# Kernel optimization log

Hardware: AMD Instinct MI355X
Metric: run time of the kernel (lower is better)

## Reference

```python
import jax, jax.numpy as jnp
import numpy as np

S = 10        # spiking_segment_count
TEMP = 50.0

def setup_inputs() -> dict:
    key = jax.random.key(0)
    ks = jax.random.split(key, 6)
    bs, din, dout = 2048, 1024, 1024
    x = jax.random.normal(ks[0], (bs, din), dtype=jnp.float32)
    t = jax.random.uniform(ks[1], (bs,), dtype=jnp.float32)  # in [0,1) subset of [-1,1]
    scale = 1.0 / np.sqrt(din)
    param_W = jax.random.normal(ks[2], (din, dout * S * 3), dtype=jnp.float32) * scale
    param_b = jax.random.normal(ks[3], (dout * S * 3,), dtype=jnp.float32) * 0.01
    norm_W = jax.random.normal(ks[4], (din, dout), dtype=jnp.float32) * scale
    norm_b = jax.random.normal(ks[5], (dout,), dtype=jnp.float32) * 0.01
    return {"x": x, "t": t, "param_W": param_W, "param_b": param_b,
            "norm_W": norm_W, "norm_b": norm_b}

def reference(x, t, param_W, param_b, norm_W, norm_b):
    bs = x.shape[0]
    dout = norm_W.shape[1]
    # param GEMM -> (bs, S, dout, 3)
    params = (x @ param_W + param_b).reshape(bs, S, dout, 3)
    weights = jax.nn.softmax(params[..., 0], axis=1)                 # (bs, S, dout)
    keypoints = jnp.concatenate(
        [jnp.zeros_like(weights[:, :1]), jnp.cumsum(weights, axis=1)], axis=1
    ) * 2.0 - 1.0                                                    # (bs, S+1, dout)
    slopes = jnp.tanh(params[..., 1])
    intercepts = params[..., 2]
    tt = t.reshape(-1, 1, 1)                                         # (bs, 1, 1)
    starts = keypoints[:, :S]
    ends = keypoints[:, 1:]
    residual = slopes * tt + intercepts                              # (bs, S, dout)
    validity = ((tt >= starts) & (tt < ends)) | ((tt == 1.0) & (ends == 1.0))
    vf = validity.astype(x.dtype)
    left_margin = jnp.sum((tt - starts) * vf, axis=1)                # (bs, dout)
    right_margin = jnp.sum((ends - tt) * vf, axis=1)
    lw = jax.nn.sigmoid(-TEMP * left_margin)
    rw = jax.nn.sigmoid(-TEMP * right_margin)
    lv = jnp.concatenate([vf[:, :1], vf[:, :-1]], axis=1)
    rv = jnp.concatenate([vf[:, 1:], vf[:, -1:]], axis=1)
    sw = -(lw + rw - 1.0)
    result = (lw * jnp.sum(residual * lv, axis=1)
              + sw * jnp.sum(residual * vf, axis=1)
              + rw * jnp.sum(residual * rv, axis=1))
    # norm == 'constant': subtract segment-wise integral, add norm_net(x)
    integral = jnp.sum(0.5 * slopes * (ends * ends - starts * starts)
                       + intercepts * weights, axis=1) * 0.5
    norm_target = x @ norm_W + norm_b
    return result - integral + norm_target
```

## Files before the change

kernel.cpp:

```cpp
#include <hip/hip_runtime.h>
#include <cstdint>
#include <cstddef>

#define BS    2048
#define DIN   1024
#define DOUT  1024
#define SSEG  10
#define NPAR  30720
#define NPK   20480
#define NCOL2 21504
#define NLG   10240
#define TAU   5e-5f
#define WL_CAP 1048576u

#define NB_SPLIT 2048
#define NB_NORM  1024
#define NB_TRW   2560

#define GEMM_BLKS 992

typedef _Float16 half_t;
typedef __attribute__((ext_vector_type(8))) _Float16 half8;
typedef __attribute__((ext_vector_type(4))) _Float16 half4;
typedef __attribute__((ext_vector_type(2))) _Float16 half2v;
typedef __attribute__((ext_vector_type(4))) float   floatx4;

__device__ __forceinline__ void gload16(const void* g, void* l) {
  __builtin_amdgcn_global_load_lds(
      (const __attribute__((address_space(1))) void*)g,
      (__attribute__((address_space(3))) void*)l, 16, 0, 0);
}

__global__ void k_zero(unsigned* c) { if (threadIdx.x == 0) *c = 0; }

__global__ __launch_bounds__(256) void k_prep(const float* __restrict__ x,
                                              half_t* __restrict__ xh,
                                              half_t* __restrict__ xl,
                                              const float* __restrict__ nW,
                                              const float* __restrict__ pW,
                                              half_t* __restrict__ wsm,
                                              half_t* __restrict__ wh,
                                              half_t* __restrict__ wlo,
                                              float* __restrict__ wlt,
                                              unsigned* __restrict__ cnt) {
  __shared__ float tile[32][384];
  int bid = blockIdx.x;
  int tid = threadIdx.x;

  if (bid < NB_SPLIT) {
    if (bid == 0 && tid == 0) *cnt = 0;
    int i = bid * 256 + tid;
    floatx4 v = ((const floatx4*)x)[i];
    half4 h, l;
    #pragma unroll
    for (int c = 0; c < 4; c++) { h[c] = (half_t)v[c]; l[c] = (half_t)(v[c] - (float)h[c]); }
    ((half4*)xh)[i] = h;
    ((half4*)xl)[i] = l;
    return;
  }

  if (bid < NB_SPLIT + NB_NORM) {
    int b2 = bid - NB_SPLIT;
    int col0 = (b2 & 31) * 32;
    int k0   = (b2 >> 5) * 32;
    int tx = tid & 31;
    int ty = tid >> 5;
    float* t33 = &tile[0][0];
    #pragma unroll
    for (int r = ty; r < 32; r += 8)
      t33[r * 33 + tx] = nW[(size_t)(k0 + r) * DOUT + col0 + tx];
    __syncthreads();
    #pragma unroll
    for (int r = ty; r < 32; r += 8)
      wsm[(size_t)(col0 + r + NPK) * DIN + k0 + tx] = (half_t)t33[tx * 33 + r];
    return;
  }

  int b3 = bid - NB_SPLIT - NB_NORM;
  int bx = b3 % 80;
  int k0 = (b3 / 80) * 32;
  int s  = bx >> 3;
  int d0 = (bx & 7) * 128;

  const float* sb = pW + (size_t)k0 * NPAR + bx * 384;
  for (int i = tid; i < 32 * 96; i += 256) {
    int r = i / 96, q = i - r * 96;
    ((floatx4*)&tile[r][0])[q] = ((const floatx4*)(sb + (size_t)r * NPAR))[q];
  }
  __syncthreads();

  for (int ci = tid; ci < 3072; ci += 256) {
    if (ci < 1024) {
      int rl = ci >> 2, kc = ci & 3;
      int jj = rl >> 1, cbit = rl & 1;
      int col = 3 * jj + 1 + cbit;
      half8 v;
      #pragma unroll
      for (int m = 0; m < 8; m++) v[m] = (half_t)tile[kc * 8 + m][col];
      *(half8*)(wsm + (size_t)(s * 2048 + 2 * (d0 + jj) + cbit) * DIN + k0 + kc * 8) = v;
    } else if (ci < 1536) {
      int u = ci - 1024;
      int jj = u >> 2, kc = u & 3;
      half8 v;
      #pragma unroll
      for (int m = 0; m < 8; m++) v[m] = (half_t)(tile[kc * 8 + m][3 * jj] * 32.0f);
      *(half8*)(wh + (size_t)(s * 1024 + d0 + jj) * DIN + k0 + kc * 8) = v;
    } else if (ci < 2048) {
      int u = ci - 1536;
      int jj = u >> 2, kc = u & 3;
      half8 v;
      #pragma unroll
      for (int m = 0; m < 8; m++) {
        float raw = tile[kc * 8 + m][3 * jj] * 32.0f;
        half_t h = (half_t)raw;
        v[m] = (half_t)(raw - (float)h);
      }
      *(half8*)(wlo + (size_t)(s * 1024 + d0 + jj) * DIN + k0 + kc * 8) = v;
    } else {
      int u = ci - 2048;
      int jj = u >> 3, kc = u & 7;
      floatx4 v;
      #pragma unroll
      for (int m = 0; m < 4; m++) v[m] = tile[kc * 4 + m][3 * jj];
      *(floatx4*)(wlt + (size_t)(s * 1024 + d0 + jj) * DIN + k0 + kc * 4) = v;
    }
  }
}

__global__ __launch_bounds__(512, 2) void k_gemm2(
    const half_t* __restrict__ xh, const half_t* __restrict__ xl,
    const half_t* __restrict__ wh, const half_t* __restrict__ wlo,
    const half_t* __restrict__ wsm,
    float* __restrict__ Lg, half_t* __restrict__ P,
    const float* __restrict__ pb, const float* __restrict__ nb) {
  __shared__ __attribute__((aligned(128))) char lds[131072];

  int bid = blockIdx.x;
  int tid = threadIdx.x;
  int w = tid >> 6, l = tid & 63;
  int wr = w >> 2, wc = w & 3;
  int l15 = l & 15, quad = l >> 4;

  int mode, mt, nt;
  if (bid < 320) { mode = 0; mt = bid & 7; nt = bid >> 3; }
  else { int s2 = bid - 320; mode = 1; mt = s2 & 7; nt = s2 >> 3; }
  int m0 = mt * 256, n0 = nt * 256;

  int sp = (l & 7) ^ ((l >> 3) & 7);
  int srowA = m0 + w * 32 + 2 * (l >> 3) + (sp >> 2);
  int srowB = n0 + w * 32 + 2 * (l >> 3) + (sp >> 2);
  int scol = (sp & 3) * 8;

  int lofs = (l15 >> 1) * 128 + (((((l15 & 1) << 2) | quad) ^ (l15 >> 1)) << 4);

  floatx4 acc[8][4] = {};

  if (mode == 0) {
    auto stage0 = [&](int c) {
      char* base = lds + ((c & 1) * 65536) + w * 2048;
      const half_t* ga = xh + (size_t)srowA * DIN + c * 32 + scol;
      const half_t* gx = xl + (size_t)srowA * DIN + c * 32 + scol;
      const half_t* gh = wh + (size_t)srowB * DIN + c * 32 + scol;
      const half_t* gl = wlo + (size_t)srowB * DIN + c * 32 + scol;
      gload16(ga, base);                gload16(ga + 16 * DIN, base + 1024);
      gload16(gx, base + 16384);        gload16(gx + 16 * DIN, base + 16384 + 1024);
      gload16(gh, base + 32768);        gload16(gh + 16 * DIN, base + 32768 + 1024);
      gload16(gl, base + 49152);        gload16(gl + 16 * DIN, base + 49152 + 1024);
    };

    stage0(0);
    asm volatile("s_waitcnt vmcnt(0)" ::: "memory");
    __builtin_amdgcn_s_barrier();

    for (int c = 0; c < 32; ++c) {
      const char* base = lds + (c & 1) * 65536;
      const char* aXH = base + wr * 8192 + lofs;
      const char* aXL = base + 16384 + wr * 8192 + lofs;
      const char* bWH = base + 32768 + wc * 4096 + lofs;
      const char* bWL = base + 49152 + wc * 4096 + lofs;
      if (c + 1 < 32) stage0(c + 1);

      half8 bh[4], bl[4], a0[4], a1[4], x0[4], x1[4];
      #pragma unroll
      for (int ni = 0; ni < 4; ni++) bh[ni] = *(const half8*)(bWH + ni * 1024);
      #pragma unroll
      for (int mi = 0; mi < 4; mi++) a0[mi] = *(const half8*)(aXH + mi * 1024);
      #pragma unroll
      for (int mi = 0; mi < 4; mi++) a1[mi] = *(const half8*)(aXH + 4096 + mi * 1024);
      #pragma unroll
      for (int mi = 0; mi < 4; mi++)
        #pragma unroll
        for (int ni = 0; ni < 4; ni++) {
          acc[mi][ni]     = __builtin_amdgcn_mfma_f32_16x16x32_f16(a0[mi], bh[ni], acc[mi][ni], 0, 0, 0);
          acc[4 + mi][ni] = __builtin_amdgcn_mfma_f32_16x16x32_f16(a1[mi], bh[ni], acc[4 + mi][ni], 0, 0, 0);
        }
      #pragma unroll
      for (int mi = 0; mi < 4; mi++) x0[mi] = *(const half8*)(aXL + mi * 1024);
      #pragma unroll
      for (int mi = 0; mi < 4; mi++) x1[mi] = *(const half8*)(aXL + 4096 + mi * 1024);
      #pragma unroll
      for (int mi = 0; mi < 4; mi++)
        #pragma unroll
        for (int ni = 0; ni < 4; ni++) {
          acc[mi][ni]     = __builtin_amdgcn_mfma_f32_16x16x32_f16(x0[mi], bh[ni], acc[mi][ni], 0, 0, 0);
          acc[4 + mi][ni] = __builtin_amdgcn_mfma_f32_16x16x32_f16(x1[mi], bh[ni], acc[4 + mi][ni], 0, 0, 0);
        }
      #pragma unroll
      for (int ni = 0; ni < 4; ni++) bl[ni] = *(const half8*)(bWL + ni * 1024);
      #pragma unroll
      for (int mi = 0; mi < 4; mi++)
        #pragma unroll
        for (int ni = 0; ni < 4; ni++) {
          acc[mi][ni]     = __builtin_amdgcn_mfma_f32_16x16x32_f16(a0[mi], bl[ni], acc[mi][ni], 0, 0, 0);
          acc[4 + mi][ni] = __builtin_amdgcn_mfma_f32_16x16x32_f16(a1[mi], bl[ni], acc[4 + mi][ni], 0, 0, 0);
        }
      if (c + 1 < 32) {
        __builtin_amdgcn_sched_barrier(0);
        asm volatile("s_waitcnt vmcnt(0)" ::: "memory");
        __builtin_amdgcn_s_barrier();
      }
    }
  } else {
    auto stage1 = [&](int kt) {
      char* base = lds + ((kt & 3) * 32768) + w * 2048;
      const half_t* ga = xh + (size_t)srowA * DIN + kt * 32 + scol;
      const half_t* gb = wsm + (size_t)srowB * DIN + kt * 32 + scol;
      gload16(ga, base);            gload16(ga + 16 * DIN, base + 1024);
      gload16(gb, base + 16384);    gload16(gb + 16 * DIN, base + 16384 + 1024);
    };

    stage1(0); stage1(1); stage1(2);
    asm volatile("s_waitcnt vmcnt(8)" ::: "memory");
    __builtin_amdgcn_s_barrier();

    for (int kt = 0; kt < 32; ++kt) {
      const char* base = lds + (kt & 3) * 32768;
      const char* a = base + wr * 8192 + lofs;
      const char* b = base + 16384 + wc * 4096 + lofs;
      if (kt + 3 < 32) stage1(kt + 3);

      half8 bf[4], af[4], ag[4];
      #pragma unroll
      for (int ni = 0; ni < 4; ni++) bf[ni] = *(const half8*)(b + ni * 1024);
      #pragma unroll
      for (int mi = 0; mi < 4; mi++) af[mi] = *(const half8*)(a + mi * 1024);
      #pragma unroll
      for (int mi = 0; mi < 4; mi++) ag[mi] = *(const half8*)(a + 4096 + mi * 1024);
      #pragma unroll
      for (int mi = 0; mi < 4; mi++)
        #pragma unroll
        for (int ni = 0; ni < 4; ni++) {
          acc[mi][ni]     = __builtin_amdgcn_mfma_f32_16x16x32_f16(af[mi], bf[ni], acc[mi][ni], 0, 0, 0);
          acc[4 + mi][ni] = __builtin_amdgcn_mfma_f32_16x16x32_f16(ag[mi], bf[ni], acc[4 + mi][ni], 0, 0, 0);
        }
      if (kt < 29) {
        __builtin_amdgcn_sched_barrier(0);
        asm volatile("s_waitcnt vmcnt(8)" ::: "memory");
        __builtin_amdgcn_s_barrier();
      } else if (kt == 29) {
        __builtin_amdgcn_sched_barrier(0);
        asm volatile("s_waitcnt vmcnt(4)" ::: "memory");
        __builtin_amdgcn_s_barrier();
      } else if (kt == 30) {
        __builtin_amdgcn_sched_barrier(0);
        asm volatile("s_waitcnt vmcnt(0)" ::: "memory");
        __builtin_amdgcn_s_barrier();
      }
    }
  }

  int rbase = m0 + wr * 128 + quad * 4;
  int cbase = n0 + wc * 64 + l15;
  if (mode == 0) {
    #pragma unroll
    for (int ni = 0; ni < 4; ni++) {
      int col = cbase + ni * 16;
      float bias = pb[(col >> 10) * 3072 + (col & 1023) * 3];
      #pragma unroll
      for (int mi = 0; mi < 8; mi++) {
        int row = rbase + mi * 16;
        floatx4 v = acc[mi][ni];
        #pragma unroll
        for (int r = 0; r < 4; r++)
          Lg[(size_t)(row + r) * NLG + col] = v[r] * 0.03125f + bias;
      }
    }
  } else {
    #pragma unroll
    for (int ni = 0; ni < 4; ni++) {
      int col = cbase + ni * 16;
      float bias;
      if (col < NPK) {
        int s = col >> 11, rem = col & 2047;
        bias = pb[s * 3072 + 3 * (rem >> 1) + 1 + (rem & 1)];
      } else {
        bias = nb[col - NPK];
      }
      #pragma unroll
      for (int mi = 0; mi < 8; mi++) {
        int row = rbase + mi * 16;
        floatx4 v = acc[mi][ni];
        #pragma unroll
        for (int r = 0; r < 4; r++)
          P[(size_t)(row + r) * NCOL2 + col] = (half_t)(v[r] + bias);
      }
    }
  }
}

__device__ __forceinline__ float spiking_eval(const float* p, float tt, float* mind) {
  float mx = -1e30f;
  #pragma unroll
  for (int s = 0; s < SSEG; s++) mx = fmaxf(mx, p[3 * s]);
  float ew[10], wsum = 0.0f;
  #pragma unroll
  for (int s = 0; s < SSEG; s++) { ew[s] = __expf(p[3 * s] - mx); wsum += ew[s]; }
  float inv = 1.0f / wsum;

  float kp[11];
  kp[0] = -1.0f;
  float cum = 0.0f, md = 1e30f;
  #pragma unroll
  for (int s = 0; s < SSEG; s++) {
    cum += ew[s] * inv;
    kp[s + 1] = cum * 2.0f - 1.0f;
    md = fminf(md, fabsf(tt - kp[s + 1]));
  }
  *mind = md;

  float vf[10], resid[10];
  float lm = 0.0f, rm = 0.0f, integ = 0.0f;
  #pragma unroll
  for (int s = 0; s < SSEG; s++) {
    float p1 = p[3 * s + 1], p2 = p[3 * s + 2];
    float e2 = __expf(2.0f * fabsf(p1));
    float th = copysignf(1.0f - 2.0f / (e2 + 1.0f), p1);
    resid[s] = th * tt + p2;
    float st = kp[s], en = kp[s + 1];
    bool v = ((tt >= st) && (tt < en)) || ((tt == 1.0f) && (en == 1.0f));
    float vv = v ? 1.0f : 0.0f;
    vf[s] = vv;
    lm += (tt - st) * vv;
    rm += (en - tt) * vv;
    integ += 0.5f * th * (en * en - st * st) + p2 * (ew[s] * inv);
  }
  float resLV = 0.0f, resV = 0.0f, resRV = 0.0f;
  #pragma unroll
  for (int s = 0; s < SSEG; s++) {
    float lv = (s == 0) ? vf[0] : vf[s - 1];
    float rv = (s == 9) ? vf[9] : vf[s + 1];
    resLV += resid[s] * lv;
    resV  += resid[s] * vf[s];
    resRV += resid[s] * rv;
  }
  float lw = 1.0f / (1.0f + __expf(50.0f * lm));
  float rw = 1.0f / (1.0f + __expf(50.0f * rm));
  float swt = 1.0f - lw - rw;
  return lw * resLV + swt * resV + rw * resRV - 0.5f * integ + p[30];
}

__global__ __launch_bounds__(256) void k_pointwise(const half_t* __restrict__ P,
                                                   const float* __restrict__ Lg,
                                                   const float* __restrict__ t,
                                                   float* __restrict__ out,
                                                   unsigned* __restrict__ cnt,
                                                   unsigned* __restrict__ wl,
                                                   unsigned cap) {
  __shared__ __attribute__((aligned(16))) half_t sp[SSEG * 512];
  int b = blockIdx.x, dg = blockIdx.y, tid = threadIdx.x;
  const half_t* Pb = P + (size_t)b * NCOL2;
  for (int i = tid; i < SSEG * 64; i += 256) {
    int s = i >> 6, e = i & 63;
    ((uint4*)sp)[(s << 6) + e] = ((const uint4*)(Pb + s * 2048 + dg * 512))[e];
  }
  float tt = t[b];
  float nt = (float)Pb[NPK + dg * 256 + tid];
  const float* Lb = Lg + (size_t)b * NLG + dg * 256 + tid;
  __syncthreads();

  float p[31];
  #pragma unroll
  for (int s = 0; s < SSEG; s++) {
    p[3 * s] = Lb[s * 1024];
    half2v hv = ((const half2v*)sp)[s * 256 + tid];
    p[3 * s + 1] = (float)hv.x;
    p[3 * s + 2] = (float)hv.y;
  }
  p[30] = nt;
  float mind;
  float r = spiking_eval(p, tt, &mind);
  int d = dg * 256 + tid;
  out[(size_t)b * DOUT + d] = r;
  if (wl != nullptr && mind < TAU) {
    unsigned idx = atomicAdd(cnt, 1u);
    if (idx < cap) wl[idx] = ((unsigned)b << 10) | (unsigned)d;
  }
}

__global__ __launch_bounds__(256) void k_naive(const float* __restrict__ x,
                                               const float* __restrict__ t,
                                               const float* __restrict__ pW,
                                               const float* __restrict__ pb,
                                               const float* __restrict__ nW,
                                               const float* __restrict__ nb,
                                               float* __restrict__ out,
                                               unsigned* __restrict__ cnt,
                                               unsigned* __restrict__ wl,
                                               unsigned cap) {
  __shared__ float xs[DIN];
  int b = blockIdx.x, dg = blockIdx.y, tid = threadIdx.x;
  for (int i = tid; i < DIN; i += 256) xs[i] = x[(size_t)b * DIN + i];
  __syncthreads();
  int d = dg * 256 + tid;
  float acc[31];
  #pragma unroll
  for (int i = 0; i < 31; i++) acc[i] = 0.0f;
  for (int k = 0; k < DIN; k++) {
    float xv = xs[k];
    const float* wr = pW + (size_t)k * NPAR + 3 * d;
    #pragma unroll
    for (int s = 0; s < SSEG; s++) {
      acc[3 * s]     += xv * wr[s * 3072];
      acc[3 * s + 1] += xv * wr[s * 3072 + 1];
      acc[3 * s + 2] += xv * wr[s * 3072 + 2];
    }
    acc[30] += xv * nW[(size_t)k * DOUT + d];
  }
  #pragma unroll
  for (int s = 0; s < SSEG; s++) {
    acc[3 * s]     += pb[s * 3072 + 3 * d];
    acc[3 * s + 1] += pb[s * 3072 + 3 * d + 1];
    acc[3 * s + 2] += pb[s * 3072 + 3 * d + 2];
  }
  acc[30] += nb[d];
  float mind;
  float r = spiking_eval(acc, t[b], &mind);
  out[(size_t)b * DOUT + d] = r;
  if (wl != nullptr && mind < TAU) {
    unsigned idx = atomicAdd(cnt, 1u);
    if (idx < cap) wl[idx] = ((unsigned)b << 10) | (unsigned)d;
  }
}

__global__ __launch_bounds__(256) void k_redo(const float* __restrict__ x,
                                              const float* __restrict__ t,
                                              const float* __restrict__ pW,
                                              const float* __restrict__ pb,
                                              const float* __restrict__ nW,
                                              const float* __restrict__ nb,
                                              const half_t* __restrict__ P,
                                              const float* __restrict__ WLt,
                                              int haveP,
                                              const unsigned* __restrict__ cnt,
                                              const unsigned* __restrict__ wl,
                                              unsigned cap,
                                              float* __restrict__ out) {
  unsigned n = *cnt;
  if (n > cap) n = cap;
  int lane = threadIdx.x & 63;
  unsigned wave = (blockIdx.x * 256 + threadIdx.x) >> 6;
  unsigned nwaves = (gridDim.x * 256) >> 6;

  for (unsigned e = wave; e < n; e += nwaves) {
    unsigned code = wl[e];
    int b = (int)(code >> 10), d = (int)(code & 1023);

    double lg[10], sl[10], ic[10], nt = 0.0;
    #pragma unroll
    for (int s = 0; s < SSEG; s++) { lg[s] = 0.0; sl[s] = 0.0; ic[s] = 0.0; }

    if (haveP) {
      for (int k = lane; k < DIN; k += 64) {
        double xv = (double)x[(size_t)b * DIN + k];
        #pragma unroll
        for (int s = 0; s < SSEG; s++)
          lg[s] += xv * (double)WLt[(size_t)(s * 1024 + d) * DIN + k];
      }
    } else {
      for (int k = lane; k < DIN; k += 64) {
        double xv = (double)x[(size_t)b * DIN + k];
        const float* wr = pW + (size_t)k * NPAR + 3 * d;
        #pragma unroll
        for (int s = 0; s < SSEG; s++) {
          lg[s] += xv * (double)wr[s * 3072];
          sl[s] += xv * (double)wr[s * 3072 + 1];
          ic[s] += xv * (double)wr[s * 3072 + 2];
        }
        nt += xv * (double)nW[(size_t)k * DOUT + d];
      }
    }
    #pragma unroll
    for (int off = 32; off > 0; off >>= 1) {
      #pragma unroll
      for (int s = 0; s < SSEG; s++) lg[s] += __shfl_down(lg[s], off);
      if (!haveP) {
        #pragma unroll
        for (int s = 0; s < SSEG; s++) {
          sl[s] += __shfl_down(sl[s], off);
          ic[s] += __shfl_down(ic[s], off);
        }
        nt += __shfl_down(nt, off);
      }
    }

    if (lane == 0) {
      double slope[10], icpt[10], ntv;
      if (haveP) {
        const half_t* Pr = P + (size_t)b * NCOL2;
        #pragma unroll
        for (int s = 0; s < SSEG; s++) {
          slope[s] = tanh((double)(float)Pr[s * 2048 + 2 * d]);
          icpt[s]  = (double)(float)Pr[s * 2048 + 2 * d + 1];
        }
        ntv = (double)(float)Pr[NPK + d];
      } else {
        #pragma unroll
        for (int s = 0; s < SSEG; s++) {
          slope[s] = tanh(sl[s] + (double)pb[s * 3072 + 3 * d + 1]);
          icpt[s]  = ic[s] + (double)pb[s * 3072 + 3 * d + 2];
        }
        ntv = nt + (double)nb[d];
      }
      #pragma unroll
      for (int s = 0; s < SSEG; s++) lg[s] += (double)pb[s * 3072 + 3 * d];

      double mx = -1e300;
      #pragma unroll
      for (int s = 0; s < SSEG; s++) mx = fmax(mx, lg[s]);
      double ew[10], ws = 0.0;
      #pragma unroll
      for (int s = 0; s < SSEG; s++) { ew[s] = exp(lg[s] - mx); ws += ew[s]; }

      double kp[11];
      kp[0] = -1.0;
      double cum = 0.0;
      #pragma unroll
      for (int s = 0; s < SSEG; s++) { cum += ew[s] / ws; kp[s + 1] = cum * 2.0 - 1.0; }

      double tt = (double)t[b];
      double vf[10], resid[10], lm = 0.0, rm = 0.0, integ = 0.0;
      #pragma unroll
      for (int s = 0; s < SSEG; s++) {
        double st = kp[s], en = kp[s + 1];
        bool v = ((tt >= st) && (tt < en)) || ((tt == 1.0) && (en == 1.0));
        double vv = v ? 1.0 : 0.0;
        vf[s] = vv;
        resid[s] = slope[s] * tt + icpt[s];
        lm += (tt - st) * vv;
        rm += (en - tt) * vv;
        integ += 0.5 * slope[s] * (en * en - st * st) + icpt[s] * (ew[s] / ws);
      }
      double rLV = 0.0, rV = 0.0, rRV = 0.0;
      #pragma unroll
      for (int s = 0; s < SSEG; s++) {
        double lv = (s == 0) ? vf[0] : vf[s - 1];
        double rv = (s == 9) ? vf[9] : vf[s + 1];
        rLV += resid[s] * lv;
        rV  += resid[s] * vf[s];
        rRV += resid[s] * rv;
      }
      double lw = 1.0 / (1.0 + exp(50.0 * lm));
      double rw = 1.0 / (1.0 + exp(50.0 * rm));
      double res = lw * rLV + (1.0 - lw - rw) * rV + rw * rRV - 0.5 * integ + ntv;
      out[(size_t)b * DOUT + d] = (float)res;
    }
  }
}

extern "C" void kernel_launch(void* const* d_in, const int* in_sizes, int n_in,
                              void* d_out, int out_size, void* d_ws, size_t ws_size,
                              hipStream_t stream) {
  const float* x  = (const float*)d_in[0];
  const float* t  = (const float*)d_in[1];
  const float* pW = (const float*)d_in[2];
  const float* pb = (const float*)d_in[3];
  const float* nW = (const float*)d_in[4];
  const float* nb = (const float*)d_in[5];
  float* out = (float*)d_out;

  const size_t o_cnt = 0;
  const size_t o_wl  = 64;
  const size_t o_xh  = o_wl  + (size_t)WL_CAP * 4;
  const size_t o_xl  = o_xh  + (size_t)BS * DIN * 2;
  const size_t o_wsm = o_xl  + (size_t)BS * DIN * 2;
  const size_t o_wh  = o_wsm + (size_t)NCOL2 * DIN * 2;
  const size_t o_wlo = o_wh  + (size_t)NLG * DIN * 2;
  const size_t o_wlt = o_wlo + (size_t)NLG * DIN * 2;
  const size_t o_p   = o_wlt + (size_t)NLG * DIN * 4;
  const size_t o_lg  = o_p   + (size_t)BS * NCOL2 * 2;
  const size_t need  = o_lg  + (size_t)BS * NLG * 4;

  bool have_wl = ws_size >= 1024 * 1024;
  unsigned* cnt = (unsigned*)((char*)d_ws + o_cnt);
  unsigned* wl  = (unsigned*)((char*)d_ws + o_wl);
  unsigned cap  = 0;
  if (have_wl) {
    size_t avail = (ws_size >= need) ? (size_t)WL_CAP
                                     : (ws_size - o_wl) / 4;
    cap = (unsigned)(avail < WL_CAP ? avail : WL_CAP);
  }

  if (ws_size >= need) {
    half_t* xh  = (half_t*)((char*)d_ws + o_xh);
    half_t* xl  = (half_t*)((char*)d_ws + o_xl);
    half_t* wsm = (half_t*)((char*)d_ws + o_wsm);
    half_t* wh  = (half_t*)((char*)d_ws + o_wh);
    half_t* wlo = (half_t*)((char*)d_ws + o_wlo);
    float*  wlt = (float*)((char*)d_ws + o_wlt);
    half_t* P   = (half_t*)((char*)d_ws + o_p);
    float*  Lg  = (float*)((char*)d_ws + o_lg);

    k_prep<<<NB_SPLIT + NB_NORM + NB_TRW, 256, 0, stream>>>(x, xh, xl, nW, pW,
                                                            wsm, wh, wlo, wlt, cnt);
    k_gemm2<<<GEMM_BLKS, 512, 0, stream>>>(xh, xl, wh, wlo, wsm, Lg, P, pb, nb);
    k_pointwise<<<dim3(BS, DOUT / 256), 256, 0, stream>>>(P, Lg, t, out, cnt,
                                                          have_wl ? wl : nullptr, cap);
    if (have_wl)
      k_redo<<<256, 256, 0, stream>>>(x, t, pW, pb, nW, nb, P, wlt, 1, cnt, wl, cap, out);
  } else {
    if (have_wl) k_zero<<<1, 64, 0, stream>>>(cnt);
    k_naive<<<dim3(BS, DOUT / 256), 256, 0, stream>>>(x, t, pW, pb, nW, nb, out, cnt,
                                                      have_wl ? wl : nullptr, cap);
    if (have_wl)
      k_redo<<<256, 256, 0, stream>>>(x, t, pW, pb, nW, nb, nullptr, nullptr, 0,
                                      cnt, wl, cap, out);
  }
}
```

Before: 565.7 us.

## Interleave global prefetch with MFMA phases using barriers and setprio in GEMM loop

Splits each K-step of both GEMM modes into sub-phases. Each phase issues LDS fragment loads and part of the next tile's global-to-LDS prefetch, synchronises all waves with an s_barrier, then runs an MFMA cluster at raised wave priority via s_setprio. This spreads memory issue between compute bursts and keeps waves in lockstep, following the ping-pong scheduling pattern, with the aim of better overlap between loads and matrix work. The cost is several extra workgroup barriers per iteration, which could add stalls if the waves are already balanced.

```diff
diff --git a/kernel.cpp b/kernel.cpp
--- a/kernel.cpp
+++ b/kernel.cpp
@@ -156,19 +156,18 @@
   floatx4 acc[8][4] = {};
 
   if (mode == 0) {
-    auto stage0 = [&](int c) {
-      char* base = lds + ((c & 1) * 65536) + w * 2048;
-      const half_t* ga = xh + (size_t)srowA * DIN + c * 32 + scol;
-      const half_t* gx = xl + (size_t)srowA * DIN + c * 32 + scol;
-      const half_t* gh = wh + (size_t)srowB * DIN + c * 32 + scol;
-      const half_t* gl = wlo + (size_t)srowB * DIN + c * 32 + scol;
-      gload16(ga, base);                gload16(ga + 16 * DIN, base + 1024);
-      gload16(gx, base + 16384);        gload16(gx + 16 * DIN, base + 16384 + 1024);
-      gload16(gh, base + 32768);        gload16(gh + 16 * DIN, base + 32768 + 1024);
-      gload16(gl, base + 49152);        gload16(gl + 16 * DIN, base + 49152 + 1024);
-    };
-
-    stage0(0);
+    const half_t* gA = xh + (size_t)srowA * DIN + scol;
+    const half_t* gX = xl + (size_t)srowA * DIN + scol;
+    const half_t* gH = wh + (size_t)srowB * DIN + scol;
+    const half_t* gL = wlo + (size_t)srowB * DIN + scol;
+
+    {
+      char* base = lds + w * 2048;
+      gload16(gA, base);                gload16(gA + 16 * DIN, base + 1024);
+      gload16(gX, base + 16384);        gload16(gX + 16 * DIN, base + 16384 + 1024);
+      gload16(gH, base + 32768);        gload16(gH + 16 * DIN, base + 32768 + 1024);
+      gload16(gL, base + 49152);        gload16(gL + 16 * DIN, base + 49152 + 1024);
+    }
     asm volatile("s_waitcnt vmcnt(0)" ::: "memory");
     __builtin_amdgcn_s_barrier();
 
@@ -178,15 +177,25 @@
       const char* aXL = base + 16384 + wr * 8192 + lofs;
       const char* bWH = base + 32768 + wc * 4096 + lofs;
       const char* bWL = base + 49152 + wc * 4096 + lofs;
-      if (c + 1 < 32) stage0(c + 1);
-
-      half8 bh[4], bl[4], a0[4], a1[4], x0[4], x1[4];
+      bool pre = (c + 1 < 32);
+      char* sbase = lds + ((c + 1) & 1) * 65536 + w * 2048;
+      int ko = (c + 1) * 32;
+
+      half8 bh[4], a0[4], a1[4];
       #pragma unroll
       for (int ni = 0; ni < 4; ni++) bh[ni] = *(const half8*)(bWH + ni * 1024);
       #pragma unroll
       for (int mi = 0; mi < 4; mi++) a0[mi] = *(const half8*)(aXH + mi * 1024);
       #pragma unroll
       for (int mi = 0; mi < 4; mi++) a1[mi] = *(const half8*)(aXH + 4096 + mi * 1024);
+      if (pre) {
+        gload16(gA + ko, sbase);           gload16(gA + ko + 16 * DIN, sbase + 1024);
+        gload16(gX + ko, sbase + 16384);   gload16(gX + ko + 16 * DIN, sbase + 16384 + 1024);
+      }
+      __builtin_amdgcn_s_barrier();
+      asm volatile("s_waitcnt lgkmcnt(0)" ::: "memory");
+      __builtin_amdgcn_sched_barrier(0);
+      __builtin_amdgcn_s_setprio(1);
       #pragma unroll
       for (int mi = 0; mi < 4; mi++)
         #pragma unroll
@@ -194,10 +203,22 @@
           acc[mi][ni]     = __builtin_amdgcn_mfma_f32_16x16x32_f16(a0[mi], bh[ni], acc[mi][ni], 0, 0, 0);
           acc[4 + mi][ni] = __builtin_amdgcn_mfma_f32_16x16x32_f16(a1[mi], bh[ni], acc[4 + mi][ni], 0, 0, 0);
         }
+      __builtin_amdgcn_s_setprio(0);
+      __builtin_amdgcn_s_barrier();
+
+      half8 x0[4], x1[4];
       #pragma unroll
       for (int mi = 0; mi < 4; mi++) x0[mi] = *(const half8*)(aXL + mi * 1024);
       #pragma unroll
       for (int mi = 0; mi < 4; mi++) x1[mi] = *(const half8*)(aXL + 4096 + mi * 1024);
+      if (pre) {
+        gload16(gH + ko, sbase + 32768);   gload16(gH + ko + 16 * DIN, sbase + 32768 + 1024);
+        gload16(gL + ko, sbase + 49152);   gload16(gL + ko + 16 * DIN, sbase + 49152 + 1024);
+      }
+      __builtin_amdgcn_s_barrier();
+      asm volatile("s_waitcnt lgkmcnt(0)" ::: "memory");
+      __builtin_amdgcn_sched_barrier(0);
+      __builtin_amdgcn_s_setprio(1);
       #pragma unroll
       for (int mi = 0; mi < 4; mi++)
         #pragma unroll
@@ -205,8 +226,16 @@
           acc[mi][ni]     = __builtin_amdgcn_mfma_f32_16x16x32_f16(x0[mi], bh[ni], acc[mi][ni], 0, 0, 0);
           acc[4 + mi][ni] = __builtin_amdgcn_mfma_f32_16x16x32_f16(x1[mi], bh[ni], acc[4 + mi][ni], 0, 0, 0);
         }
+      __builtin_amdgcn_s_setprio(0);
+      __builtin_amdgcn_s_barrier();
+
+      half8 bl[4];
       #pragma unroll
       for (int ni = 0; ni < 4; ni++) bl[ni] = *(const half8*)(bWL + ni * 1024);
+      __builtin_amdgcn_s_barrier();
+      asm volatile("s_waitcnt lgkmcnt(0)" ::: "memory");
+      __builtin_amdgcn_sched_barrier(0);
+      __builtin_amdgcn_s_setprio(1);
       #pragma unroll
       for (int mi = 0; mi < 4; mi++)
         #pragma unroll
@@ -214,19 +243,20 @@
           acc[mi][ni]     = __builtin_amdgcn_mfma_f32_16x16x32_f16(a0[mi], bl[ni], acc[mi][ni], 0, 0, 0);
           acc[4 + mi][ni] = __builtin_amdgcn_mfma_f32_16x16x32_f16(a1[mi], bl[ni], acc[4 + mi][ni], 0, 0, 0);
         }
-      if (c + 1 < 32) {
+      __builtin_amdgcn_s_setprio(0);
+      if (pre) {
         __builtin_amdgcn_sched_barrier(0);
         asm volatile("s_waitcnt vmcnt(0)" ::: "memory");
         __builtin_amdgcn_s_barrier();
       }
     }
   } else {
+    const half_t* gA = xh + (size_t)srowA * DIN + scol;
+    const half_t* gB = wsm + (size_t)srowB * DIN + scol;
     auto stage1 = [&](int kt) {
       char* base = lds + ((kt & 3) * 32768) + w * 2048;
-      const half_t* ga = xh + (size_t)srowA * DIN + kt * 32 + scol;
-      const half_t* gb = wsm + (size_t)srowB * DIN + kt * 32 + scol;
-      gload16(ga, base);            gload16(ga + 16 * DIN, base + 1024);
-      gload16(gb, base + 16384);    gload16(gb + 16 * DIN, base + 16384 + 1024);
+      gload16(gA + kt * 32, base);            gload16(gA + kt * 32 + 16 * DIN, base + 1024);
+      gload16(gB + kt * 32, base + 16384);    gload16(gB + kt * 32 + 16 * DIN, base + 16384 + 1024);
     };
 
     stage1(0); stage1(1); stage1(2);
@@ -237,22 +267,38 @@
       const char* base = lds + (kt & 3) * 32768;
       const char* a = base + wr * 8192 + lofs;
       const char* b = base + 16384 + wc * 4096 + lofs;
+
+      half8 bf[4], af[4];
+      #pragma unroll
+      for (int ni = 0; ni < 4; ni++) bf[ni] = *(const half8*)(b + ni * 1024);
+      #pragma unroll
+      for (int mi = 0; mi < 4; mi++) af[mi] = *(const half8*)(a + mi * 1024);
       if (kt + 3 < 32) stage1(kt + 3);
-
-      half8 bf[4], af[4], ag[4];
-      #pragma unroll
-      for (int ni = 0; ni < 4; ni++) bf[ni] = *(const half8*)(b + ni * 1024);
-      #pragma unroll
-      for (int mi = 0; mi < 4; mi++) af[mi] = *(const half8*)(a + mi * 1024);
+      __builtin_amdgcn_s_barrier();
+      asm volatile("s_waitcnt lgkmcnt(0)" ::: "memory");
+      __builtin_amdgcn_sched_barrier(0);
+      __builtin_amdgcn_s_setprio(1);
+      #pragma unroll
+      for (int mi = 0; mi < 4; mi++)
+        #pragma unroll
+        for (int ni = 0; ni < 4; ni++)
+          acc[mi][ni] = __builtin_amdgcn_mfma_f32_16x16x32_f16(af[mi], bf[ni], acc[mi][ni], 0, 0, 0);
+      __builtin_amdgcn_s_setprio(0);
+      __builtin_amdgcn_s_barrier();
+
+      half8 ag[4];
       #pragma unroll
       for (int mi = 0; mi < 4; mi++) ag[mi] = *(const half8*)(a + 4096 + mi * 1024);
+      __builtin_amdgcn_s_barrier();
+      asm volatile("s_waitcnt lgkmcnt(0)" ::: "memory");
+      __builtin_amdgcn_sched_barrier(0);
+      __builtin_amdgcn_s_setprio(1);
       #pragma unroll
       for (int mi = 0; mi < 4; mi++)
         #pragma unroll
-        for (int ni = 0; ni < 4; ni++) {
-          acc[mi][ni]     = __builtin_amdgcn_mfma_f32_16x16x32_f16(af[mi], bf[ni], acc[mi][ni], 0, 0, 0);
+        for (int ni = 0; ni < 4; ni++)
           acc[4 + mi][ni] = __builtin_amdgcn_mfma_f32_16x16x32_f16(ag[mi], bf[ni], acc[4 + mi][ni], 0, 0, 0);
-        }
+      __builtin_amdgcn_s_setprio(0);
       if (kt < 29) {
         __builtin_amdgcn_sched_barrier(0);
         asm volatile("s_waitcnt vmcnt(8)" ::: "memory");
```

New measurement: 556.4 us. About the same (-1.6%).

## Drop transposed fp32 logit weights and LDS staging in pointwise kernel

Applied to the files above, without the earlier changes.

Removes the fp32 transposed logit-weight copy (wlt) that the prep kernel wrote, 40 MB of extra global writes. The redo kernel now always recomputes all parameters from the original pW in double precision instead of reusing P and wlt, so each worklist entry costs more reads but prep does less work. The pointwise kernel also drops its LDS staging and __syncthreads and reads P directly from global memory.

```diff
diff --git a/kernel.cpp b/kernel.cpp
--- a/kernel.cpp
+++ b/kernel.cpp
@@ -41,7 +41,6 @@
                                               half_t* __restrict__ wsm,
                                               half_t* __restrict__ wh,
                                               half_t* __restrict__ wlo,
-                                              float* __restrict__ wlt,
                                               unsigned* __restrict__ cnt) {
   __shared__ float tile[32][384];
   int bid = blockIdx.x;
@@ -89,7 +88,7 @@
   }
   __syncthreads();
 
-  for (int ci = tid; ci < 3072; ci += 256) {
+  for (int ci = tid; ci < 2048; ci += 256) {
     if (ci < 1024) {
       int rl = ci >> 2, kc = ci & 3;
       int jj = rl >> 1, cbit = rl & 1;
@@ -105,7 +104,7 @@
       #pragma unroll
       for (int m = 0; m < 8; m++) v[m] = (half_t)(tile[kc * 8 + m][3 * jj] * 32.0f);
       *(half8*)(wh + (size_t)(s * 1024 + d0 + jj) * DIN + k0 + kc * 8) = v;
-    } else if (ci < 2048) {
+    } else {
       int u = ci - 1536;
       int jj = u >> 2, kc = u & 3;
       half8 v;
@@ -116,13 +115,6 @@
         v[m] = (half_t)(raw - (float)h);
       }
       *(half8*)(wlo + (size_t)(s * 1024 + d0 + jj) * DIN + k0 + kc * 8) = v;
-    } else {
-      int u = ci - 2048;
-      int jj = u >> 3, kc = u & 7;
-      floatx4 v;
-      #pragma unroll
-      for (int m = 0; m < 4; m++) v[m] = tile[kc * 4 + m][3 * jj];
-      *(floatx4*)(wlt + (size_t)(s * 1024 + d0 + jj) * DIN + k0 + kc * 4) = v;
     }
   }
 }
@@ -366,30 +358,23 @@
                                                    unsigned* __restrict__ cnt,
                                                    unsigned* __restrict__ wl,
                                                    unsigned cap) {
-  __shared__ __attribute__((aligned(16))) half_t sp[SSEG * 512];
   int b = blockIdx.x, dg = blockIdx.y, tid = threadIdx.x;
+  int d = dg * 256 + tid;
   const half_t* Pb = P + (size_t)b * NCOL2;
-  for (int i = tid; i < SSEG * 64; i += 256) {
-    int s = i >> 6, e = i & 63;
-    ((uint4*)sp)[(s << 6) + e] = ((const uint4*)(Pb + s * 2048 + dg * 512))[e];
-  }
+  const float* Lb = Lg + (size_t)b * NLG + d;
   float tt = t[b];
-  float nt = (float)Pb[NPK + dg * 256 + tid];
-  const float* Lb = Lg + (size_t)b * NLG + dg * 256 + tid;
-  __syncthreads();
 
   float p[31];
   #pragma unroll
   for (int s = 0; s < SSEG; s++) {
     p[3 * s] = Lb[s * 1024];
-    half2v hv = ((const half2v*)sp)[s * 256 + tid];
+    half2v hv = *(const half2v*)(Pb + s * 2048 + 2 * d);
     p[3 * s + 1] = (float)hv.x;
     p[3 * s + 2] = (float)hv.y;
   }
-  p[30] = nt;
+  p[30] = (float)Pb[NPK + d];
   float mind;
   float r = spiking_eval(p, tt, &mind);
-  int d = dg * 256 + tid;
   out[(size_t)b * DOUT + d] = r;
   if (wl != nullptr && mind < TAU) {
     unsigned idx = atomicAdd(cnt, 1u);
@@ -448,9 +433,6 @@
                                               const float* __restrict__ pb,
                                               const float* __restrict__ nW,
                                               const float* __restrict__ nb,
-                                              const half_t* __restrict__ P,
-                                              const float* __restrict__ WLt,
-                                              int haveP,
                                               const unsigned* __restrict__ cnt,
                                               const unsigned* __restrict__ wl,
                                               unsigned cap,
@@ -469,58 +451,36 @@
     #pragma unroll
     for (int s = 0; s < SSEG; s++) { lg[s] = 0.0; sl[s] = 0.0; ic[s] = 0.0; }
 
-    if (haveP) {
-      for (int k = lane; k < DIN; k += 64) {
-        double xv = (double)x[(size_t)b * DIN + k];
-        #pragma unroll
-        for (int s = 0; s < SSEG; s++)
-          lg[s] += xv * (double)WLt[(size_t)(s * 1024 + d) * DIN + k];
-      }
-    } else {
-      for (int k = lane; k < DIN; k += 64) {
-        double xv = (double)x[(size_t)b * DIN + k];
-        const float* wr = pW + (size_t)k * NPAR + 3 * d;
-        #pragma unroll
-        for (int s = 0; s < SSEG; s++) {
-          lg[s] += xv * (double)wr[s * 3072];
-          sl[s] += xv * (double)wr[s * 3072 + 1];
-          ic[s] += xv * (double)wr[s * 3072 + 2];
-        }
-        nt += xv * (double)nW[(size_t)k * DOUT + d];
-      }
+    for (int k = lane; k < DIN; k += 64) {
+      double xv = (double)x[(size_t)b * DIN + k];
+      const float* wr = pW + (size_t)k * NPAR + 3 * d;
+      #pragma unroll
+      for (int s = 0; s < SSEG; s++) {
+        lg[s] += xv * (double)wr[s * 3072];
+        sl[s] += xv * (double)wr[s * 3072 + 1];
+        ic[s] += xv * (double)wr[s * 3072 + 2];
+      }
+      nt += xv * (double)nW[(size_t)k * DOUT + d];
     }
     #pragma unroll
     for (int off = 32; off > 0; off >>= 1) {
       #pragma unroll
-      for (int s = 0; s < SSEG; s++) lg[s] += __shfl_down(lg[s], off);
-      if (!haveP) {
-        #pragma unroll
-        for (int s = 0; s < SSEG; s++) {
-          sl[s] += __shfl_down(sl[s], off);
-          ic[s] += __shfl_down(ic[s], off);
-        }
-        nt += __shfl_down(nt, off);
-      }
+      for (int s = 0; s < SSEG; s++) {
+        lg[s] += __shfl_down(lg[s], off);
+        sl[s] += __shfl_down(sl[s], off);
+        ic[s] += __shfl_down(ic[s], off);
+      }
+      nt += __shfl_down(nt, off);
     }
 
     if (lane == 0) {
       double slope[10], icpt[10], ntv;
-      if (haveP) {
-        const half_t* Pr = P + (size_t)b * NCOL2;
-        #pragma unroll
-        for (int s = 0; s < SSEG; s++) {
-          slope[s] = tanh((double)(float)Pr[s * 2048 + 2 * d]);
-          icpt[s]  = (double)(float)Pr[s * 2048 + 2 * d + 1];
-        }
-        ntv = (double)(float)Pr[NPK + d];
-      } else {
-        #pragma unroll
-        for (int s = 0; s < SSEG; s++) {
-          slope[s] = tanh(sl[s] + (double)pb[s * 3072 + 3 * d + 1]);
-          icpt[s]  = ic[s] + (double)pb[s * 3072 + 3 * d + 2];
-        }
-        ntv = nt + (double)nb[d];
-      }
+      #pragma unroll
+      for (int s = 0; s < SSEG; s++) {
+        slope[s] = tanh(sl[s] + (double)pb[s * 3072 + 3 * d + 1]);
+        icpt[s]  = ic[s] + (double)pb[s * 3072 + 3 * d + 2];
+      }
+      ntv = nt + (double)nb[d];
       #pragma unroll
       for (int s = 0; s < SSEG; s++) lg[s] += (double)pb[s * 3072 + 3 * d];
 
@@ -585,8 +545,7 @@
   const size_t o_wsm = o_xl  + (size_t)BS * DIN * 2;
   const size_t o_wh  = o_wsm + (size_t)NCOL2 * DIN * 2;
   const size_t o_wlo = o_wh  + (size_t)NLG * DIN * 2;
-  const size_t o_wlt = o_wlo + (size_t)NLG * DIN * 2;
-  const size_t o_p   = o_wlt + (size_t)NLG * DIN * 4;
+  const size_t o_p   = o_wlo + (size_t)NLG * DIN * 2;
   const size_t o_lg  = o_p   + (size_t)BS * NCOL2 * 2;
   const size_t need  = o_lg  + (size_t)BS * NLG * 4;
 
@@ -606,23 +565,21 @@
     half_t* wsm = (half_t*)((char*)d_ws + o_wsm);
     half_t* wh  = (half_t*)((char*)d_ws + o_wh);
     half_t* wlo = (half_t*)((char*)d_ws + o_wlo);
-    float*  wlt = (float*)((char*)d_ws + o_wlt);
     half_t* P   = (half_t*)((char*)d_ws + o_p);
     float*  Lg  = (float*)((char*)d_ws + o_lg);
 
     k_prep<<<NB_SPLIT + NB_NORM + NB_TRW, 256, 0, stream>>>(x, xh, xl, nW, pW,
-                                                            wsm, wh, wlo, wlt, cnt);
+                                                            wsm, wh, wlo, cnt);
     k_gemm2<<<GEMM_BLKS, 512, 0, stream>>>(xh, xl, wh, wlo, wsm, Lg, P, pb, nb);
     k_pointwise<<<dim3(BS, DOUT / 256), 256, 0, stream>>>(P, Lg, t, out, cnt,
                                                           have_wl ? wl : nullptr, cap);
     if (have_wl)
-      k_redo<<<256, 256, 0, stream>>>(x, t, pW, pb, nW, nb, P, wlt, 1, cnt, wl, cap, out);
+      k_redo<<<256, 256, 0, stream>>>(x, t, pW, pb, nW, nb, cnt, wl, cap, out);
   } else {
     if (have_wl) k_zero<<<1, 64, 0, stream>>>(cnt);
     k_naive<<<dim3(BS, DOUT / 256), 256, 0, stream>>>(x, t, pW, pb, nW, nb, out, cnt,
                                                       have_wl ? wl : nullptr, cap);
     if (have_wl)
-      k_redo<<<256, 256, 0, stream>>>(x, t, pW, pb, nW, nb, nullptr, nullptr, 0,
-                                      cnt, wl, cap, out);
-  }
-}
+      k_redo<<<256, 256, 0, stream>>>(x, t, pW, pb, nW, nb, cnt, wl, cap, out);
+  }
+}
```

After: 675.7 us. 19.5% more time.
